# Performance work log

Measured on AMD Instinct MI355X. Metric: run time of the kernel, lower is better.

The kernel has to match this reference:

```python
import jax, jax.numpy as jnp
import numpy as np


def _pairwise_upper_dists(x):
    # x: [N, D] -> distances for all i<j pairs, shape [N*(N-1)/2]
    n = x.shape[0]
    sq = jnp.sum(x * x, axis=-1)                      # [N]
    d2 = sq[:, None] + sq[None, :] - 2.0 * (x @ x.T)  # [N, N]
    d2 = jnp.maximum(d2, 0.0)
    iu, ju = jnp.triu_indices(n, k=1)                 # matches combinations(range(n), 2)
    return jnp.sqrt(d2[iu, ju])


def setup_inputs() -> dict:
    key = jax.random.key(0)
    k1, k2 = jax.random.split(key)
    pred = jax.random.normal(k1, (1024, 8192), dtype=jnp.float32)
    target = jax.random.normal(k2, (1024, 8192), dtype=jnp.float32)
    return {"pred": pred, "target": target}


def reference(pred, target):
    # all_pairs_in_batch=True branch: Euclidean distance per pair, MSE between
    # the pred-distance vector and the target-distance vector.
    pred_d = _pairwise_upper_dists(pred)      # [P]
    target_d = _pairwise_upper_dists(target)  # [P]
    return jnp.mean((pred_d - target_d) ** 2)
```

## Files before the change

kernel.cpp:

```cpp
#include <hip/hip_runtime.h>
#include <hip/hip_bf16.h>
#include <hip/hip_fp16.h>

#define D 8192
#define NPAIR 523776.0

typedef short short8 __attribute__((ext_vector_type(8)));
typedef float f32x4 __attribute__((ext_vector_type(4)));
typedef _Float16 f16x8 __attribute__((ext_vector_type(8)));
typedef int int32x4 __attribute__((ext_vector_type(4)));

__device__ __forceinline__ short8 cvt8(const float4 a, const float4 b) {
    union { short8 s; __hip_bfloat162 h[4]; } u;
    u.h[0] = __float22bfloat162_rn(make_float2(a.x, a.y));
    u.h[1] = __float22bfloat162_rn(make_float2(a.z, a.w));
    u.h[2] = __float22bfloat162_rn(make_float2(b.x, b.y));
    u.h[3] = __float22bfloat162_rn(make_float2(b.z, b.w));
    return u.s;
}

__device__ __forceinline__ int q8(float x) {
    return __float2int_rn(fminf(fmaxf(x * 32.f, -127.f), 127.f));
}
__device__ __forceinline__ int pack4(float a, float b, float c, float d) {
    return (q8(a) & 255) | ((q8(b) & 255) << 8) | ((q8(c) & 255) << 16) | ((q8(d) & 255) << 24);
}

__device__ __forceinline__ void decode_bid(int bid, int& m, int& ti, int& tj, int& k0, int& nsteps) {
    int x = bid & 7, s = bid >> 3;
    m = x >> 2;
    int xr = x & 3;
    if (s < 16) {
        ti = tj = s & 7;
        int c = ((s >> 3) << 2) + xr;
        k0 = c * 1024; nsteps = 16;
    } else {
        int sp = s - 16;
        int c = (sp / 28) * 4 + xr;
        int tt = sp % 28;
        int a = 0;
        while (tt >= 7 - a) { tt -= 7 - a; ++a; }
        ti = a; tj = a + 1 + tt;
        k0 = c * 512; nsteps = 8;
    }
}
__device__ __forceinline__ int bid_off(int m, int tt, int c) {
    return (m * 4 + (c & 3)) + ((16 + (c >> 2) * 28 + tt) << 3);
}
__device__ __forceinline__ int bid_diag(int m, int dt, int c) {
    return (m * 4 + (c & 3)) + ((((c >> 2) << 3) + dt) << 3);
}

__global__ __launch_bounds__(256)
void convert_kernel(const float* __restrict__ pred, const float* __restrict__ tgt,
                    char* __restrict__ q) {
    const int idx = blockIdx.x * 256 + threadIdx.x;
    const int t = idx & 511;
    const int c = idx >> 9;
    const int m = c >> 10, p = (c >> 7) & 7, ks = c & 127;
    const int rl = t >> 2;
    const int s = (t & 3) ^ ((rl >> 1) & 3);
    const float* __restrict__ src = (m ? tgt : pred) + (size_t)(p * 128 + rl) * D + ks * 64 + s * 16;
    const float4 a = ((const float4*)src)[0];
    const float4 b = ((const float4*)src)[1];
    const float4 e = ((const float4*)src)[2];
    const float4 f = ((const float4*)src)[3];
    int32x4 o;
    o[0] = pack4(a.x, a.y, a.z, a.w);
    o[1] = pack4(b.x, b.y, b.z, b.w);
    o[2] = pack4(e.x, e.y, e.z, e.w);
    o[3] = pack4(f.x, f.y, f.z, f.w);
    *(int32x4*)(q + (size_t)c * 8192 + t * 16) = o;
}

#define LOADSTEP(S, RA, RB) { \
    const char* pa_ = gAc + (size_t)(S) * 8192; \
    RA[0] = *(const int32x4*)(pa_ + rbA + kby); \
    RA[1] = *(const int32x4*)(pa_ + rbA + 1024 + kby); \
    RA[2] = *(const int32x4*)(pa_ + rbA + 2048 + kby); \
    RA[3] = *(const int32x4*)(pa_ + rbA + 3072 + kby); \
    const char* pb_ = gBc + (size_t)(S) * 8192; \
    RB[0] = *(const int32x4*)(pb_ + rbB + kby); \
    RB[1] = *(const int32x4*)(pb_ + rbB + 1024 + kby); \
}

#define MFMASTEP(RA, RB) { \
    _Pragma("unroll") \
    for (int mi = 0; mi < 4; ++mi) { \
        acc[mi][0] = __builtin_amdgcn_mfma_i32_16x16x64_i8(RA[mi], RB[0], acc[mi][0], 0, 0, 0); \
        acc[mi][1] = __builtin_amdgcn_mfma_i32_16x16x64_i8(RA[mi], RB[1], acc[mi][1], 0, 0, 0); \
    } \
}

__global__ __launch_bounds__(512, 4)
void gram_kernel(const char* __restrict__ q, __half* __restrict__ part,
                 float* __restrict__ norms) {
    int m, ti, tj, k0, nsteps;
    decode_bid(blockIdx.x, m, ti, tj, k0, nsteps);
    const bool same = (ti == tj);

    __shared__ short ls[16384];
    char* lsb = (char*)ls;

    const int tid = threadIdx.x;
    const int lane = tid & 63;
    const int wid = tid >> 6;
    const int wr = wid >> 2, wc = wid & 3;

    const char* __restrict__ gAc = q + (size_t)(m * 1024 + ti * 128 + (k0 >> 6)) * 8192;
    const char* __restrict__ gBc = q + (size_t)(m * 1024 + tj * 128 + (k0 >> 6)) * 8192;

    const int rbA = (wr * 64 + (lane & 15)) * 64;
    const int rbB = (wc * 32 + (lane & 15)) * 64;
    const int kby = (((lane >> 4) ^ (((lane & 15) >> 1) & 3)) << 4);

    int32x4 zero = {0, 0, 0, 0};
    int32x4 acc[4][2];
#pragma unroll
    for (int mi = 0; mi < 4; ++mi) { acc[mi][0] = zero; acc[mi][1] = zero; }

    int32x4 aX[4], bX[2], aY[4], bY[2];
    LOADSTEP(0, aX, bX)
    LOADSTEP(1, aY, bY)
    for (int sp = 0; sp + 2 < nsteps; sp += 2) {
        MFMASTEP(aX, bX)
        LOADSTEP(sp + 2, aX, bX)
        MFMASTEP(aY, bY)
        if (sp + 3 < nsteps) LOADSTEP(sp + 3, aY, bY)
    }
    MFMASTEP(aX, bX)
    MFMASTEP(aY, bY)

    if (same) {
#pragma unroll
        for (int mi = 0; mi < 4; ++mi)
#pragma unroll
            for (int ni = 0; ni < 2; ++ni)
#pragma unroll
                for (int r = 0; r < 4; ++r) {
                    int li = wr * 64 + mi * 16 + (lane >> 4) * 4 + r;
                    int lj = wc * 32 + ni * 16 + (lane & 15);
                    if (li == lj)
                        atomicAdd(&norms[m * 1024 + ti * 128 + li],
                                  (float)acc[mi][ni][r] * (1.f / 1024.f));
                }
    }
#pragma unroll
    for (int mi = 0; mi < 4; ++mi)
#pragma unroll
        for (int ni = 0; ni < 2; ++ni)
#pragma unroll
            for (int r = 0; r < 4; ++r) {
                int li = wr * 64 + mi * 16 + (lane >> 4) * 4 + r;
                int lj = wc * 32 + ni * 16 + (lane & 15);
                int byte = li * 256 + ((lj * 2) ^ ((li & 7) << 4));
                *(__half*)(lsb + byte) = __float2half_rn((float)acc[mi][ni][r] * (1.f / 1024.f));
            }
    __syncthreads();
    char* __restrict__ dstb = (char*)(part + (size_t)blockIdx.x * 16384);
#pragma unroll
    for (int qq = 0; qq < 4; ++qq) {
        int L = qq * 8192 + tid * 16;
        int li = L >> 8;
        f16x8 v = *(const f16x8*)(lsb + (L ^ ((li & 7) << 4)));
        *(f16x8*)(dstb + L) = v;
    }
}

__global__ __launch_bounds__(256)
void loss_store_kernel(const __half* __restrict__ part, const float* __restrict__ norms,
                       float* __restrict__ partial) {
    const int tid = threadIdx.x;
    const int sid = blockIdx.x * 256 + tid;
    const int i  = sid >> 7;
    const int j0 = (sid & 127) << 3;
    float local = 0.f;
    if (j0 + 7 > i) {
        const int ti = i >> 7, tj = j0 >> 7;
        const int el = ((i & 127) << 7) + (j0 & 127);
        float gp[8] = {0,0,0,0,0,0,0,0}, gt[8] = {0,0,0,0,0,0,0,0};
        if (ti == tj) {
#pragma unroll
            for (int c = 0; c < 8; ++c) {
                f16x8 vp = *(const f16x8*)(part + (size_t)bid_diag(0, ti, c) * 16384 + el);
                f16x8 vt = *(const f16x8*)(part + (size_t)bid_diag(1, ti, c) * 16384 + el);
#pragma unroll
                for (int e = 0; e < 8; ++e) { gp[e] += (float)vp[e]; gt[e] += (float)vt[e]; }
            }
        } else {
            int tt = 7 * ti - (ti * (ti - 1)) / 2 + (tj - ti - 1);
#pragma unroll
            for (int c = 0; c < 16; ++c) {
                f16x8 vp = *(const f16x8*)(part + (size_t)bid_off(0, tt, c) * 16384 + el);
                f16x8 vt = *(const f16x8*)(part + (size_t)bid_off(1, tt, c) * 16384 + el);
#pragma unroll
                for (int e = 0; e < 8; ++e) { gp[e] += (float)vp[e]; gt[e] += (float)vt[e]; }
            }
        }
        const float nip = norms[i], nit = norms[1024 + i];
        const float4 njp0 = *(const float4*)(norms + j0);
        const float4 njp1 = *(const float4*)(norms + j0 + 4);
        const float4 njt0 = *(const float4*)(norms + 1024 + j0);
        const float4 njt1 = *(const float4*)(norms + 1024 + j0 + 4);
        const float njp[8] = {njp0.x, njp0.y, njp0.z, njp0.w, njp1.x, njp1.y, njp1.z, njp1.w};
        const float njt[8] = {njt0.x, njt0.y, njt0.z, njt0.w, njt1.x, njt1.y, njt1.z, njt1.w};
#pragma unroll
        for (int e = 0; e < 8; ++e) {
            int j = j0 + e;
            if (j > i) {
                float dp = nip + njp[e] - 2.f * gp[e];
                float dt = nit + njt[e] - 2.f * gt[e];
                float c2 = sqrtf(fmaxf(dp, 0.f)) - sqrtf(fmaxf(dt, 0.f));
                local += c2 * c2;
            }
        }
    }
#pragma unroll
    for (int off = 32; off > 0; off >>= 1) local += __shfl_down(local, off);
    __shared__ float wsum[4];
    if ((tid & 63) == 0) wsum[tid >> 6] = local;
    __syncthreads();
    if (tid == 0) partial[blockIdx.x] = wsum[0] + wsum[1] + wsum[2] + wsum[3];
}

template<int NPART>
__global__ __launch_bounds__(256)
void finalize_kernel(const float* __restrict__ partial, float* __restrict__ out) {
    const int tid = threadIdx.x;
    double local = 0.0;
#pragma unroll
    for (int k = 0; k < NPART / 256; ++k) local += (double)partial[tid + k * 256];
#pragma unroll
    for (int off = 32; off > 0; off >>= 1) local += __shfl_down(local, off);
    __shared__ double wsum[4];
    if ((tid & 63) == 0) wsum[tid >> 6] = local;
    __syncthreads();
    if (tid == 0) out[0] = (float)((wsum[0] + wsum[1] + wsum[2] + wsum[3]) / NPAIR);
}

__device__ __forceinline__ void decode_bid_fb(int bid, int& m, int& ti, int& tj, int& k0, int& nsteps) {
    int x = bid & 7, s = bid >> 3;
    m = x >> 2;
    int xr = x & 3;
    if (s < 16) {
        ti = tj = s & 7;
        int c = ((s >> 3) << 2) + xr;
        k0 = c * 1024; nsteps = 32;
    } else {
        int sp = s - 16;
        int c = (sp / 28) * 4 + xr;
        int tt = sp % 28;
        int a = 0;
        while (tt >= 7 - a) { tt -= 7 - a; ++a; }
        ti = a; tj = a + 1 + tt;
        k0 = c * 512; nsteps = 16;
    }
}

__global__ __launch_bounds__(512)
void gram_fb(const float* __restrict__ pred, const float* __restrict__ tgt,
             float* __restrict__ g4) {
    int m, ti, tj, k0, nsteps;
    decode_bid_fb(blockIdx.x, m, ti, tj, k0, nsteps);
    const bool same = (ti == tj);
    const float* __restrict__ x = m ? tgt : pred;
    __shared__ short lsA[2][4096];
    __shared__ short lsB[2][4096];
    const int tid = threadIdx.x;
    const int lane = tid & 63;
    const int wid = tid >> 6;
    const int wr = wid >> 2, wc = wid & 3;
    const int srow = tid >> 2, sc8 = tid & 3;
    const float* __restrict__ gA = x + (size_t)(ti * 128 + srow) * D + k0 + sc8 * 8;
    const float* __restrict__ gB = x + (size_t)(tj * 128 + srow) * D + k0 + sc8 * 8;
    const int wby = srow * 64 + ((sc8 ^ ((srow >> 1) & 3)) << 4);
    const int rbA = (wr * 64 + (lane & 15)) * 64;
    const int rbB = (wc * 32 + (lane & 15)) * 64;
    const int kby = (((lane >> 4) ^ (((lane & 15) >> 1) & 3)) << 4);
    f32x4 zero = {0.f, 0.f, 0.f, 0.f};
    f32x4 acc[4][2];
#pragma unroll
    for (int mi = 0; mi < 4; ++mi) { acc[mi][0] = zero; acc[mi][1] = zero; }
    float4 ra0, ra1, rb0, rb1;
    { const float4* p = (const float4*)gA; ra0 = p[0]; ra1 = p[1];
      if (!same) { const float4* qq = (const float4*)gB; rb0 = qq[0]; rb1 = qq[1]; } }
    *(short8*)((char*)lsA[0] + wby) = cvt8(ra0, ra1);
    if (!same) *(short8*)((char*)lsB[0] + wby) = cvt8(rb0, rb1);
    { const float4* p = (const float4*)(gA + 32); ra0 = p[0]; ra1 = p[1];
      if (!same) { const float4* qq = (const float4*)(gB + 32); rb0 = qq[0]; rb1 = qq[1]; } }
    asm volatile("s_waitcnt lgkmcnt(0)" ::: "memory");
    __builtin_amdgcn_s_barrier();
    for (int step = 0; step < nsteps; ++step) {
        const int cur = step & 1;
        const short* __restrict__ bufA = lsA[cur];
        const short* __restrict__ bufB = same ? lsA[cur] : lsB[cur];
        short8 bf0 = *(const short8*)((const char*)bufB + (rbB + kby));
        short8 bf1 = *(const short8*)((const char*)bufB + (rbB + 1024 + kby));
#pragma unroll
        for (int mi = 0; mi < 4; ++mi) {
            short8 af = *(const short8*)((const char*)bufA + (rbA + mi * 1024 + kby));
            acc[mi][0] = __builtin_amdgcn_mfma_f32_16x16x32_bf16(af, bf0, acc[mi][0], 0, 0, 0);
            acc[mi][1] = __builtin_amdgcn_mfma_f32_16x16x32_bf16(af, bf1, acc[mi][1], 0, 0, 0);
        }
        if (step + 1 < nsteps) {
            const int nxt = cur ^ 1;
            *(short8*)((char*)lsA[nxt] + wby) = cvt8(ra0, ra1);
            if (!same) *(short8*)((char*)lsB[nxt] + wby) = cvt8(rb0, rb1);
            if (step + 2 < nsteps) {
                const float4* p = (const float4*)(gA + (step + 2) * 32);
                ra0 = p[0]; ra1 = p[1];
                if (!same) { const float4* qq = (const float4*)(gB + (step + 2) * 32); rb0 = qq[0]; rb1 = qq[1]; }
            }
        }
        asm volatile("s_waitcnt lgkmcnt(0)" ::: "memory");
        __builtin_amdgcn_s_barrier();
    }
#pragma unroll
    for (int mi = 0; mi < 4; ++mi)
#pragma unroll
        for (int ni = 0; ni < 2; ++ni)
#pragma unroll
            for (int r = 0; r < 4; ++r) {
                int gi = ti * 128 + wr * 64 + mi * 16 + (lane >> 4) * 4 + r;
                int gj = tj * 128 + wc * 32 + ni * 16 + (lane & 15);
                atomicAdd(&g4[(size_t)m * 1048576 + gi * 1024 + gj], acc[mi][ni][r]);
            }
}

__global__ __launch_bounds__(256)
void loss_atomic_kernel(const float* __restrict__ gram, float* __restrict__ partial) {
    const float* __restrict__ gP = gram;
    const float* __restrict__ gT = gram + 1024 * 1024;
    const int tid = threadIdx.x;
    const int base = blockIdx.x * 256 + tid;
    float local = 0.f;
#pragma unroll
    for (int s = 0; s < 4; ++s) {
        int lin = base + s * 262144;
        int i = lin >> 10, j = lin & 1023;
        if (j > i) {
            float dp = gP[i * 1024 + i] + gP[j * 1024 + j] - 2.f * gP[lin];
            float dt = gT[i * 1024 + i] + gT[j * 1024 + j] - 2.f * gT[lin];
            float c = sqrtf(fmaxf(dp, 0.f)) - sqrtf(fmaxf(dt, 0.f));
            local += c * c;
        }
    }
#pragma unroll
    for (int off = 32; off > 0; off >>= 1) local += __shfl_down(local, off);
    __shared__ float wsum[4];
    if ((tid & 63) == 0) wsum[tid >> 6] = local;
    __syncthreads();
    if (tid == 0) partial[blockIdx.x] = wsum[0] + wsum[1] + wsum[2] + wsum[3];
}

extern "C" void kernel_launch(void* const* d_in, const int* in_sizes, int n_in,
                              void* d_out, int out_size, void* d_ws, size_t ws_size,
                              hipStream_t stream) {
    const float* pred = (const float*)d_in[0];
    const float* tgt  = (const float*)d_in[1];
    const size_t q_bytes    = (size_t)2048 * 8192;
    const size_t part_bytes = (size_t)1024 * 16384 * 2;
    const size_t need = q_bytes + part_bytes + (2048 + 512) * sizeof(float);
    if (ws_size >= need) {
        char* qbuf     = (char*)d_ws;
        __half* part   = (__half*)((char*)d_ws + q_bytes);
        float* norms   = (float*)((char*)part + part_bytes);
        float* partial = norms + 2048;
        hipMemsetAsync(norms, 0, 2048 * sizeof(float), stream);
        convert_kernel<<<4096, 256, 0, stream>>>(pred, tgt, qbuf);
        gram_kernel<<<1024, 512, 0, stream>>>(qbuf, part, norms);
        loss_store_kernel<<<512, 256, 0, stream>>>(part, norms, partial);
        finalize_kernel<512><<<1, 256, 0, stream>>>(partial, (float*)d_out);
    } else {
        float* gram    = (float*)d_ws;
        float* partial = (float*)d_ws + (size_t)2 * 1024 * 1024;
        hipMemsetAsync(gram, 0, (size_t)2 * 1024 * 1024 * sizeof(float), stream);
        gram_fb<<<1024, 512, 0, stream>>>(pred, tgt, gram);
        loss_atomic_kernel<<<1024, 256, 0, stream>>>(gram, partial);
        finalize_kernel<1024><<<1, 256, 0, stream>>>(partial, (float*)d_out);
    }
}
```

Measured before the change: 54.38 us.

## Fuse int8 quantization into gram kernel with LDS double-buffered staging

Drops the separate convert kernel and its quantized workspace. The gram kernel now loads fp32 rows directly, quantizes them to int8 in registers, and writes them into a double-buffered LDS tile that the MFMA loop reads. Diagonal tiles load only one operand. This removes the extra kernel launch and the global write/read round trip of the quantized data. In exchange, fp32 is re-read by multiple off-diagonal tiles, per-step barriers are added, and the occupancy hint rises to 6.

```diff
diff --git a/kernel.cpp b/kernel.cpp
--- a/kernel.cpp
+++ b/kernel.cpp
@@ -24,6 +24,15 @@
 }
 __device__ __forceinline__ int pack4(float a, float b, float c, float d) {
     return (q8(a) & 255) | ((q8(b) & 255) << 8) | ((q8(c) & 255) << 16) | ((q8(d) & 255) << 24);
+}
+__device__ __forceinline__ int32x4 qpack16(const float4 f0, const float4 f1,
+                                           const float4 f2, const float4 f3) {
+    int32x4 o;
+    o[0] = pack4(f0.x, f0.y, f0.z, f0.w);
+    o[1] = pack4(f1.x, f1.y, f1.z, f1.w);
+    o[2] = pack4(f2.x, f2.y, f2.z, f2.w);
+    o[3] = pack4(f3.x, f3.y, f3.z, f3.w);
+    return o;
 }
 
 __device__ __forceinline__ void decode_bid(int bid, int& m, int& ti, int& tj, int& k0, int& nsteps) {
@@ -51,53 +60,18 @@
     return (m * 4 + (c & 3)) + ((((c >> 2) << 3) + dt) << 3);
 }
 
-__global__ __launch_bounds__(256)
-void convert_kernel(const float* __restrict__ pred, const float* __restrict__ tgt,
-                    char* __restrict__ q) {
-    const int idx = blockIdx.x * 256 + threadIdx.x;
-    const int t = idx & 511;
-    const int c = idx >> 9;
-    const int m = c >> 10, p = (c >> 7) & 7, ks = c & 127;
-    const int rl = t >> 2;
-    const int s = (t & 3) ^ ((rl >> 1) & 3);
-    const float* __restrict__ src = (m ? tgt : pred) + (size_t)(p * 128 + rl) * D + ks * 64 + s * 16;
-    const float4 a = ((const float4*)src)[0];
-    const float4 b = ((const float4*)src)[1];
-    const float4 e = ((const float4*)src)[2];
-    const float4 f = ((const float4*)src)[3];
-    int32x4 o;
-    o[0] = pack4(a.x, a.y, a.z, a.w);
-    o[1] = pack4(b.x, b.y, b.z, b.w);
-    o[2] = pack4(e.x, e.y, e.z, e.w);
-    o[3] = pack4(f.x, f.y, f.z, f.w);
-    *(int32x4*)(q + (size_t)c * 8192 + t * 16) = o;
-}
-
-#define LOADSTEP(S, RA, RB) { \
-    const char* pa_ = gAc + (size_t)(S) * 8192; \
-    RA[0] = *(const int32x4*)(pa_ + rbA + kby); \
-    RA[1] = *(const int32x4*)(pa_ + rbA + 1024 + kby); \
-    RA[2] = *(const int32x4*)(pa_ + rbA + 2048 + kby); \
-    RA[3] = *(const int32x4*)(pa_ + rbA + 3072 + kby); \
-    const char* pb_ = gBc + (size_t)(S) * 8192; \
-    RB[0] = *(const int32x4*)(pb_ + rbB + kby); \
-    RB[1] = *(const int32x4*)(pb_ + rbB + 1024 + kby); \
-}
-
-#define MFMASTEP(RA, RB) { \
-    _Pragma("unroll") \
-    for (int mi = 0; mi < 4; ++mi) { \
-        acc[mi][0] = __builtin_amdgcn_mfma_i32_16x16x64_i8(RA[mi], RB[0], acc[mi][0], 0, 0, 0); \
-        acc[mi][1] = __builtin_amdgcn_mfma_i32_16x16x64_i8(RA[mi], RB[1], acc[mi][1], 0, 0, 0); \
-    } \
-}
-
-__global__ __launch_bounds__(512, 4)
-void gram_kernel(const char* __restrict__ q, __half* __restrict__ part,
-                 float* __restrict__ norms) {
+#define LOAD4(RR, PTR) { \
+    const float4* p_ = (const float4*)(PTR); \
+    RR[0] = p_[0]; RR[1] = p_[1]; RR[2] = p_[2]; RR[3] = p_[3]; \
+}
+
+__global__ __launch_bounds__(512, 6)
+void gram_fused(const float* __restrict__ pred, const float* __restrict__ tgt,
+                __half* __restrict__ part, float* __restrict__ norms) {
     int m, ti, tj, k0, nsteps;
     decode_bid(blockIdx.x, m, ti, tj, k0, nsteps);
     const bool same = (ti == tj);
+    const float* __restrict__ x = m ? tgt : pred;
 
     __shared__ short ls[16384];
     char* lsb = (char*)ls;
@@ -107,9 +81,13 @@
     const int wid = tid >> 6;
     const int wr = wid >> 2, wc = wid & 3;
 
-    const char* __restrict__ gAc = q + (size_t)(m * 1024 + ti * 128 + (k0 >> 6)) * 8192;
-    const char* __restrict__ gBc = q + (size_t)(m * 1024 + tj * 128 + (k0 >> 6)) * 8192;
-
+    const int srow = tid >> 2, sks = tid & 3;
+    const int sslot = sks ^ ((srow >> 1) & 3);
+    const float* __restrict__ gAs = x + (size_t)(ti * 128 + srow) * D + k0 + sslot * 16;
+    const float* __restrict__ gBs = x + (size_t)(tj * 128 + srow) * D + k0 + sslot * 16;
+    const int wbyA = srow * 64 + sks * 16;
+
+    const int boff = same ? 0 : 8192;
     const int rbA = (wr * 64 + (lane & 15)) * 64;
     const int rbB = (wc * 32 + (lane & 15)) * 64;
     const int kby = (((lane >> 4) ^ (((lane & 15) >> 1) & 3)) << 4);
@@ -119,17 +97,46 @@
 #pragma unroll
     for (int mi = 0; mi < 4; ++mi) { acc[mi][0] = zero; acc[mi][1] = zero; }
 
-    int32x4 aX[4], bX[2], aY[4], bY[2];
-    LOADSTEP(0, aX, bX)
-    LOADSTEP(1, aY, bY)
-    for (int sp = 0; sp + 2 < nsteps; sp += 2) {
-        MFMASTEP(aX, bX)
-        LOADSTEP(sp + 2, aX, bX)
-        MFMASTEP(aY, bY)
-        if (sp + 3 < nsteps) LOADSTEP(sp + 3, aY, bY)
-    }
-    MFMASTEP(aX, bX)
-    MFMASTEP(aY, bY)
+    float4 ra[4], rb[4];
+    LOAD4(ra, gAs)
+    if (!same) LOAD4(rb, gBs)
+    *(int32x4*)(lsb + wbyA) = qpack16(ra[0], ra[1], ra[2], ra[3]);
+    if (!same) *(int32x4*)(lsb + 8192 + wbyA) = qpack16(rb[0], rb[1], rb[2], rb[3]);
+    if (nsteps > 1) {
+        LOAD4(ra, gAs + 64)
+        if (!same) LOAD4(rb, gBs + 64)
+    }
+    asm volatile("s_waitcnt lgkmcnt(0)" ::: "memory");
+    __builtin_amdgcn_s_barrier();
+
+    int cC = 0, cN = 16384;
+    for (int sp = 0; sp < nsteps; ++sp) {
+        {
+            const char* __restrict__ bA = lsb + cC;
+            const char* __restrict__ bB = lsb + cC + boff;
+            __builtin_amdgcn_s_setprio(1);
+            int32x4 b0 = *(const int32x4*)(bB + rbB + kby);
+            int32x4 b1 = *(const int32x4*)(bB + rbB + 1024 + kby);
+#pragma unroll
+            for (int mi = 0; mi < 4; ++mi) {
+                int32x4 af = *(const int32x4*)(bA + rbA + mi * 1024 + kby);
+                acc[mi][0] = __builtin_amdgcn_mfma_i32_16x16x64_i8(af, b0, acc[mi][0], 0, 0, 0);
+                acc[mi][1] = __builtin_amdgcn_mfma_i32_16x16x64_i8(af, b1, acc[mi][1], 0, 0, 0);
+            }
+            __builtin_amdgcn_s_setprio(0);
+        }
+        if (sp + 1 < nsteps) {
+            *(int32x4*)(lsb + cN + wbyA) = qpack16(ra[0], ra[1], ra[2], ra[3]);
+            if (!same) *(int32x4*)(lsb + cN + 8192 + wbyA) = qpack16(rb[0], rb[1], rb[2], rb[3]);
+            if (sp + 2 < nsteps) {
+                LOAD4(ra, gAs + (sp + 2) * 64)
+                if (!same) LOAD4(rb, gBs + (sp + 2) * 64)
+            }
+        }
+        asm volatile("s_waitcnt lgkmcnt(0)" ::: "memory");
+        __builtin_amdgcn_s_barrier();
+        { int t_ = cC; cC = cN; cN = t_; }
+    }
 
     if (same) {
 #pragma unroll
@@ -358,17 +365,14 @@
                               hipStream_t stream) {
     const float* pred = (const float*)d_in[0];
     const float* tgt  = (const float*)d_in[1];
-    const size_t q_bytes    = (size_t)2048 * 8192;
     const size_t part_bytes = (size_t)1024 * 16384 * 2;
-    const size_t need = q_bytes + part_bytes + (2048 + 512) * sizeof(float);
+    const size_t need = part_bytes + (2048 + 512) * sizeof(float);
     if (ws_size >= need) {
-        char* qbuf     = (char*)d_ws;
-        __half* part   = (__half*)((char*)d_ws + q_bytes);
-        float* norms   = (float*)((char*)part + part_bytes);
+        __half* part   = (__half*)d_ws;
+        float* norms   = (float*)((char*)d_ws + part_bytes);
         float* partial = norms + 2048;
         hipMemsetAsync(norms, 0, 2048 * sizeof(float), stream);
-        convert_kernel<<<4096, 256, 0, stream>>>(pred, tgt, qbuf);
-        gram_kernel<<<1024, 512, 0, stream>>>(qbuf, part, norms);
+        gram_fused<<<1024, 512, 0, stream>>>(pred, tgt, part, norms);
         loss_store_kernel<<<512, 256, 0, stream>>>(part, norms, partial);
         finalize_kernel<512><<<1, 256, 0, stream>>>(partial, (float*)d_out);
     } else {
```

Measured after the change: 89.20 us. 1.64x slower.
